# Kernel tuning notes

Hardware: AMD Instinct MI355X
Metric: run time of the kernel (lower is better)

The kernel has to match this reference:

```python
import jax, jax.numpy as jnp
import numpy as np

B, T, D_K, N_HEADS, D_FF, VOCAB, N_LAYERS = 4, 1024, 1024, 16, 4096, 65, 6


def setup_inputs() -> dict:
    key = jax.random.key(0)
    ks = jax.random.split(key, 12)
    f = lambda k, sh: jax.random.normal(k, sh, dtype=jnp.float32) * 0.02
    return {
        "batchData": jax.random.randint(ks[0], (B, T), 0, VOCAB),
        "target": jax.random.randint(ks[1], (B, T), 0, VOCAB),
        "pos": jnp.arange(T),
        "Wtok": f(ks[2], (VOCAB, D_K)),
        "Wpos": f(ks[3], (T, D_K)),
        "Wq": f(ks[4], (D_K, D_K)), "bq": jnp.zeros((D_K,), jnp.float32),
        "Wk": f(ks[5], (D_K, D_K)), "bk": jnp.zeros((D_K,), jnp.float32),
        "Wv": f(ks[6], (D_K, D_K)), "bv": jnp.zeros((D_K,), jnp.float32),
        "W1": f(ks[7], (D_K, D_FF)), "b1": jnp.zeros((D_FF,), jnp.float32),
        "W2": f(ks[8], (D_FF, D_K)), "b2": jnp.zeros((D_K,), jnp.float32),
        "ln_w": jnp.ones((D_K,), jnp.float32),
        "Wf": f(ks[9], (D_K, VOCAB)), "bf": jnp.zeros((VOCAB,), jnp.float32),
        "n_layers": N_LAYERS,
        "n_heads": N_HEADS,
    }


def layer_norm(x, w, eps=1e-5):
    m = jnp.mean(x, axis=-1, keepdims=True)
    v = jnp.var(x, axis=-1, keepdims=True)
    return (x - m) / jnp.sqrt(v + eps) * w


def reference(batchData, target, pos, Wtok, Wpos, Wq, bq, Wk, bk, Wv, bv,
              W1, b1, W2, b2, ln_w, Wf, bf, n_layers, n_heads):
    x = Wtok[batchData] + Wpos[pos]  # [B, T, C] (pos embedding broadcasts)
    Bsz, Tlen, C = x.shape
    dh = C // n_heads
    mask = jnp.tril(jnp.ones((Tlen, Tlen), dtype=bool))
    inv_sqrt_dk = 1.0 / jnp.sqrt(jnp.float32(C))  # source divides by sqrt(full d_k)

    def block(x):
        q = (x @ Wq + bq).reshape(Bsz, Tlen, n_heads, dh).transpose(0, 2, 1, 3)
        k = (x @ Wk + bk).reshape(Bsz, Tlen, n_heads, dh).transpose(0, 2, 1, 3)
        v = (x @ Wv + bv).reshape(Bsz, Tlen, n_heads, dh).transpose(0, 2, 1, 3)
        scores = jnp.einsum('bhqd,bhkd->bhqk', q, k) * inv_sqrt_dk
        scores = jnp.where(mask, scores, -jnp.inf)
        attn = jax.nn.softmax(scores, axis=-1)
        h = jnp.einsum('bhqk,bhkd->bhqd', attn, v)
        h = h.transpose(0, 2, 1, 3).reshape(Bsz, Tlen, C)
        h = h + layer_norm(h, ln_w)           # x = x + ln(x) (shared ln)
        ff = jax.nn.relu(h @ W1 + b1) @ W2 + b2
        return ff + layer_norm(ff, ln_w)      # same shared ln again

    # ModuleList repeats the SAME block object, so weights are shared across layers
    for _ in range(n_layers):
        x = block(x)

    logits = x @ Wf + bf                       # [B, T, V]
    probs = jax.nn.softmax(logits, axis=1)     # softmax over T, as in source
    pred = probs.reshape(Bsz * Tlen, -1)
    onehot = jax.nn.one_hot(target.reshape(-1), VOCAB, dtype=jnp.float32)
    # F.cross_entropy with soft (one-hot float) targets
    loss = -jnp.mean(jnp.sum(onehot * jax.nn.log_softmax(pred, axis=-1), axis=-1))
    return loss, probs
```

## Files before the change

kernel.cpp:

```cpp
#include <hip/hip_runtime.h>

typedef __attribute__((ext_vector_type(8))) short bh8;
typedef __attribute__((ext_vector_type(4))) float f4v;

constexpr int VOC = 65;
constexpr int NL  = 6;
constexpr int Mrow = 4096;

__device__ inline float b2f(unsigned short u) {
  union { unsigned int i; float f; } x; x.i = ((unsigned int)u) << 16; return x.f;
}
__device__ inline unsigned short f2b(float f) {
  union { float f; unsigned int i; } x; x.f = f;
  return (unsigned short)((x.i + 0x7FFFu + ((x.i >> 16) & 1u)) >> 16);
}
__device__ inline unsigned char f2e4m3(float v) {
  return (unsigned char)(__builtin_amdgcn_cvt_pk_fp8_f32(v, v, 0, false) & 0xFF);
}
__device__ inline unsigned int pk4_e4m3(float a, float b, float c, float d) {
  int v = __builtin_amdgcn_cvt_pk_fp8_f32(a, b, 0, false);
  v = __builtin_amdgcn_cvt_pk_fp8_f32(c, d, v, true);
  return (unsigned int)v;
}
__device__ inline void gld16(const void* g, void* l) {
  __builtin_amdgcn_global_load_lds(
      (const __attribute__((address_space(1))) unsigned int*)g,
      (__attribute__((address_space(3))) unsigned int*)l, 16, 0, 0);
}
__device__ inline bh8 lds_swz(const unsigned short* base, int row, int colbyte) {
  int off = row * 128 + (colbyte ^ ((row & 7) << 4));
  return *(const bh8*)((const char*)base + off);
}
__device__ inline f4v mfma16(bh8 a, bh8 b, f4v c) {
  return __builtin_amdgcn_mfma_f32_16x16x32_bf16(a, b, c, 0, 0, 0);
}
__device__ inline f4v mfma8(long a, long b, f4v c) {
  return __builtin_amdgcn_mfma_f32_16x16x32_fp8_fp8(a, b, c, 0, 0, 0);
}
#define WAITV(n) asm volatile("s_waitcnt vmcnt(" #n ")" ::: "memory")
#define LGKM0 asm volatile("s_waitcnt lgkmcnt(0)" ::: "memory")
#define LGKM8 asm volatile("s_waitcnt lgkmcnt(8)" ::: "memory")
#define SBAR0 __builtin_amdgcn_sched_barrier(0)
#define BAR __builtin_amdgcn_s_barrier()

__global__ __launch_bounds__(256) void wt_conv(const float* __restrict__ src,
    unsigned short* __restrict__ dst, int K, int N) {
  __shared__ float t[32][33];
  int k0 = blockIdx.x * 32, n0 = blockIdx.y * 32;
  int tid = threadIdx.x;
#pragma unroll
  for (int i = 0; i < 4; ++i) {
    int idx = tid + i * 256;
    int kr = idx >> 5, nc = idx & 31;
    t[kr][nc] = (n0 + nc < N) ? src[(size_t)(k0 + kr) * N + n0 + nc] : 0.f;
  }
  __syncthreads();
#pragma unroll
  for (int i = 0; i < 4; ++i) {
    int idx = tid + i * 256;
    int nr = idx >> 5, kc = idx & 31;
    dst[(size_t)(n0 + nr) * K + k0 + kc] = f2b(t[kc][nr]);
  }
}

__global__ __launch_bounds__(256) void wt_conv8(const float* __restrict__ src,
    unsigned char* __restrict__ dst, int K, int N) {
  __shared__ float t[32][33];
  int k0 = blockIdx.x * 32, n0 = blockIdx.y * 32;
  int tid = threadIdx.x;
#pragma unroll
  for (int i = 0; i < 4; ++i) {
    int idx = tid + i * 256;
    int kr = idx >> 5, nc = idx & 31;
    t[kr][nc] = (n0 + nc < N) ? src[(size_t)(k0 + kr) * N + n0 + nc] : 0.f;
  }
  __syncthreads();
#pragma unroll
  for (int i = 0; i < 4; ++i) {
    int idx = tid + i * 256;
    int nr = idx >> 5, kc = idx & 31;
    dst[(size_t)(n0 + nr) * K + k0 + kc] = f2e4m3(t[kc][nr] * 16.f);
  }
}

__global__ __launch_bounds__(256) void bias_prep(
    const float* __restrict__ bq, const float* __restrict__ bk,
    const float* __restrict__ bv, const float* __restrict__ bf,
    float* __restrict__ bqkv, float* __restrict__ bfp) {
  int i = blockIdx.x * 256 + threadIdx.x;
  if (i < 1024) bqkv[i] = bq[i];
  else if (i < 2048) bqkv[i] = bk[i - 1024];
  else if (i < 3072) bqkv[i] = bv[i - 2048];
  else if (i < 3200) bfp[i - 3072] = (i - 3072 < VOC) ? bf[i - 3072] : 0.f;
}

__global__ __launch_bounds__(256) void embed_bf(const int* __restrict__ tok,
    const float* __restrict__ Wtok, const float* __restrict__ Wpos,
    unsigned short* __restrict__ Xb) {
  int bt = blockIdx.x, t = bt & 1023, tid = threadIdx.x;
  int id = tok[bt];
  float4 a = ((const float4*)(Wtok + (size_t)id * 1024))[tid];
  float4 p = ((const float4*)(Wpos + (size_t)t * 1024))[tid];
  ushort4 o;
  o.x = f2b(a.x + p.x); o.y = f2b(a.y + p.y);
  o.z = f2b(a.z + p.z); o.w = f2b(a.w + p.w);
  ((ushort4*)(Xb + (size_t)bt * 1024))[tid] = o;
}

template <bool RELU, bool PART, bool VT>
__global__ __launch_bounds__(512, 1) void gemm256(
    const unsigned short* __restrict__ A, const unsigned short* __restrict__ Bt,
    const float* __restrict__ bias, void* __restrict__ Cout,
    unsigned short* __restrict__ Vtout, long N, long Kloop, long lda, long ldb,
    int MT, int NT, int CM, int CN) {
  __shared__ unsigned short Abuf[2][256 * 64];
  __shared__ unsigned short Bbuf[2][256 * 64];
  const int tid = threadIdx.x, lane = tid & 63, w = tid >> 6;
  const int wr = w >> 2, wc = w & 3;
  const int lr = lane & 15, lh = lane >> 4, lh4 = lh * 4;

  const int x = (int)blockIdx.x & 7, j = (int)blockIdx.x >> 3;
  const int gM = MT / CM;
  const int rowT = (x % gM) * CM + (j % CM);
  const int c = (x / gM) * CN + (j / CM);
  const int colT = c % NT, ksl = c / NT;
  const long row0 = (long)rowT * 256, col0 = (long)colT * 256;
  const long kOff = (long)ksl * Kloop;

  f4v acc[8][4];
#pragma unroll
  for (int i = 0; i < 8; ++i)
#pragma unroll
    for (int jj = 0; jj < 4; ++jj) acc[i][jj] = f4v{0.f, 0.f, 0.f, 0.f};

  const int rg = tid >> 3, sIdx = tid & 7;
  const int ch = sIdx ^ (rg & 7);
  const unsigned short* Ap = A + (row0 + rg) * lda + kOff + ch * 8;
  const unsigned short* Bp = Bt + (col0 + rg) * ldb + kOff + ch * 8;

  auto stA = [&](int t, int h) {
    const long k0 = (long)t << 6;
#pragma unroll
    for (int i = 0; i < 2; ++i)
      gld16(Ap + (long)(h * 128 + i * 64) * lda + k0,
            &Abuf[t & 1][(h * 128 + i * 64) * 64 + tid * 8]);
  };
  auto stB = [&](int t, int h) {
    const long k0 = (long)t << 6;
#pragma unroll
    for (int i = 0; i < 2; ++i)
      gld16(Bp + (long)(h * 128 + i * 64) * ldb + k0,
            &Bbuf[t & 1][(h * 128 + i * 64) * 64 + tid * 8]);
  };

  const int nt = (int)(Kloop >> 6);
  stA(0, 0); stA(0, 1); stB(0, 0); stB(0, 1);
  stA(1, 0); stA(1, 1); stB(1, 0);
  WAITV(6);
  BAR;

  const int sl0 = (lh ^ (lr & 7)) * 8;
  const int sl1 = ((4 + lh) ^ (lr & 7)) * 8;

  for (int t = 0; t < nt; ++t) {
    const unsigned short* Ab = Abuf[t & 1];
    const unsigned short* Bb = Bbuf[t & 1];
    bh8 a0[4][2], a1[4][2], b0[2][2], b1[2][2];
#pragma unroll
    for (int mi = 0; mi < 4; ++mi) {
      const int row = (2 * mi + wr) * 16 + lr;
      a0[mi][0] = *(const bh8*)&Ab[row * 64 + sl0];
      a0[mi][1] = *(const bh8*)&Ab[row * 64 + sl1];
    }
#pragma unroll
    for (int ni = 0; ni < 2; ++ni) {
      const int row = (4 * ni + wc) * 16 + lr;
      b0[ni][0] = *(const bh8*)&Bb[row * 64 + sl0];
      b0[ni][1] = *(const bh8*)&Bb[row * 64 + sl1];
    }
    if (t + 1 < nt) stB(t + 1, 1);
    LGKM8;
    BAR;
    LGKM0; SBAR0;
    __builtin_amdgcn_s_setprio(1);
#pragma unroll
    for (int mi = 0; mi < 4; ++mi)
#pragma unroll
      for (int ni = 0; ni < 2; ++ni) {
        acc[mi][ni] = mfma16(a0[mi][0], b0[ni][0], acc[mi][ni]);
        acc[mi][ni] = mfma16(a0[mi][1], b0[ni][1], acc[mi][ni]);
      }
    __builtin_amdgcn_s_setprio(0);
    BAR;
#pragma unroll
    for (int mi = 0; mi < 4; ++mi) {
      const int row = (2 * (mi + 4) + wr) * 16 + lr;
      a1[mi][0] = *(const bh8*)&Ab[row * 64 + sl0];
      a1[mi][1] = *(const bh8*)&Ab[row * 64 + sl1];
    }
    if (t + 2 < nt) stA(t + 2, 0);
    BAR;
    LGKM0; SBAR0;
    __builtin_amdgcn_s_setprio(1);
#pragma unroll
    for (int mi = 0; mi < 4; ++mi)
#pragma unroll
      for (int ni = 0; ni < 2; ++ni) {
        acc[mi + 4][ni] = mfma16(a1[mi][0], b0[ni][0], acc[mi + 4][ni]);
        acc[mi + 4][ni] = mfma16(a1[mi][1], b0[ni][1], acc[mi + 4][ni]);
      }
    __builtin_amdgcn_s_setprio(0);
    BAR;
#pragma unroll
    for (int ni = 0; ni < 2; ++ni) {
      const int row = (4 * (ni + 2) + wc) * 16 + lr;
      b1[ni][0] = *(const bh8*)&Bb[row * 64 + sl0];
      b1[ni][1] = *(const bh8*)&Bb[row * 64 + sl1];
    }
    if (t + 2 < nt) stA(t + 2, 1);
    BAR;
    LGKM0; SBAR0;
    __builtin_amdgcn_s_setprio(1);
#pragma unroll
    for (int mi = 0; mi < 4; ++mi)
#pragma unroll
      for (int ni = 0; ni < 2; ++ni) {
        acc[mi][ni + 2] = mfma16(a0[mi][0], b1[ni][0], acc[mi][ni + 2]);
        acc[mi][ni + 2] = mfma16(a0[mi][1], b1[ni][1], acc[mi][ni + 2]);
      }
    __builtin_amdgcn_s_setprio(0);
    BAR;
    if (t + 2 < nt) stB(t + 2, 0);
    BAR;
    SBAR0;
    __builtin_amdgcn_s_setprio(1);
#pragma unroll
    for (int mi = 0; mi < 4; ++mi)
#pragma unroll
      for (int ni = 0; ni < 2; ++ni) {
        acc[mi + 4][ni + 2] = mfma16(a1[mi][0], b1[ni][0], acc[mi + 4][ni + 2]);
        acc[mi + 4][ni + 2] = mfma16(a1[mi][1], b1[ni][1], acc[mi + 4][ni + 2]);
      }
    __builtin_amdgcn_s_setprio(0);
    if (t + 1 < nt) {
      if (t + 2 < nt) { WAITV(6); } else { WAITV(0); }
      BAR;
    }
  }

  if (PART) {
    unsigned short* P = (unsigned short*)Cout + (size_t)ksl * 4096 * 1024;
#pragma unroll
    for (int mi = 0; mi < 8; ++mi)
#pragma unroll
      for (int ni = 0; ni < 4; ++ni) {
        long col = col0 + (4 * ni + wc) * 16 + lr;
#pragma unroll
        for (int r = 0; r < 4; ++r) {
          long row = row0 + (2 * mi + wr) * 16 + lh4 + r;
          P[row * N + col] = f2b(acc[mi][ni][r]);
        }
      }
    return;
  }
  if (VT && col0 >= 2048) {
#pragma unroll
    for (int mi = 0; mi < 8; ++mi)
#pragma unroll
      for (int ni = 0; ni < 4; ++ni) {
        int col = (int)col0 + (4 * ni + wc) * 16 + lr;
        float bb = bias[col];
        int cc = col - 2048;
        long row = row0 + (2 * mi + wr) * 16 + lh4;
        int bi = (int)(row >> 10), tt = (int)(row & 1023);
        ushort4 o;
        o.x = f2b(acc[mi][ni][0] + bb);
        o.y = f2b(acc[mi][ni][1] + bb);
        o.z = f2b(acc[mi][ni][2] + bb);
        o.w = f2b(acc[mi][ni][3] + bb);
        *(ushort4*)&Vtout[((size_t)(bi * 16 + (cc >> 6)) * 64 + (cc & 63)) *
                              1024 + tt] = o;
      }
    return;
  }
#pragma unroll
  for (int mi = 0; mi < 8; ++mi)
#pragma unroll
    for (int ni = 0; ni < 4; ++ni) {
      long col = col0 + (4 * ni + wc) * 16 + lr;
      float bb = bias[col];
      const float qsc = (VT && col < 1024) ? 0.03125f : 1.0f;
#pragma unroll
      for (int r = 0; r < 4; ++r) {
        long row = row0 + (2 * mi + wr) * 16 + lh4 + r;
        float v = acc[mi][ni][r] + bb;
        if (VT) v *= qsc;
        if (RELU) v = fmaxf(v, 0.f);
        ((unsigned short*)Cout)[row * N + col] = f2b(v);
      }
    }
}

template <bool PART>
__global__ __launch_bounds__(512, 1) void gemm256f8(
    const unsigned char* __restrict__ A, const unsigned char* __restrict__ Bt,
    const float* __restrict__ bias, void* __restrict__ Cout,
    long N, long Kloop, long lda, long ldb, int MT, int NT, int CM, int CN) {
  __shared__ unsigned char Abuf[2][256 * 128];
  __shared__ unsigned char Bbuf[2][256 * 128];
  const int tid = threadIdx.x, lane = tid & 63, w = tid >> 6;
  const int wr = w >> 2, wc = w & 3;
  const int lr = lane & 15, lh = lane >> 4, lh4 = lh * 4;

  const int x = (int)blockIdx.x & 7, j = (int)blockIdx.x >> 3;
  const int gM = MT / CM;
  const int rowT = (x % gM) * CM + (j % CM);
  const int c = (x / gM) * CN + (j / CM);
  const int colT = c % NT, ksl = c / NT;
  const long row0 = (long)rowT * 256, col0 = (long)colT * 256;
  const long kOff = (long)ksl * Kloop;

  f4v acc[8][4];
#pragma unroll
  for (int i = 0; i < 8; ++i)
#pragma unroll
    for (int jj = 0; jj < 4; ++jj) acc[i][jj] = f4v{0.f, 0.f, 0.f, 0.f};

  const int rg = tid >> 3, sIdx = tid & 7;
  const int ch = sIdx ^ (rg & 7);
  const unsigned char* Ap = A + (row0 + rg) * lda + kOff + ch * 16;
  const unsigned char* Bp = Bt + (col0 + rg) * ldb + kOff + ch * 16;

  auto stA = [&](int t, int h) {
    const long k0 = (long)t << 7;
#pragma unroll
    for (int i = 0; i < 2; ++i)
      gld16(Ap + (long)(h * 128 + i * 64) * lda + k0,
            &Abuf[t & 1][(h * 128 + i * 64) * 128 + tid * 16]);
  };
  auto stB = [&](int t, int h) {
    const long k0 = (long)t << 7;
#pragma unroll
    for (int i = 0; i < 2; ++i)
      gld16(Bp + (long)(h * 128 + i * 64) * ldb + k0,
            &Bbuf[t & 1][(h * 128 + i * 64) * 128 + tid * 16]);
  };

  const int nt = (int)(Kloop >> 7);
  stA(0, 0); stA(0, 1); stB(0, 0); stB(0, 1);
  stA(1, 0); stA(1, 1); stB(1, 0);
  WAITV(6);
  BAR;

  int fsl[4];
#pragma unroll
  for (int ks = 0; ks < 4; ++ks)
    fsl[ks] = (((ks * 2 + (lh >> 1)) ^ (lr & 7)) << 4) + (lh & 1) * 8;

  for (int t = 0; t < nt; ++t) {
    const unsigned char* Ab = Abuf[t & 1];
    const unsigned char* Bb = Bbuf[t & 1];
    long a0[4][4], a1[4][4], b0[2][4], b1[2][4];
#pragma unroll
    for (int mi = 0; mi < 4; ++mi) {
      const unsigned char* rp = &Ab[((2 * mi + wr) * 16 + lr) * 128];
#pragma unroll
      for (int ks = 0; ks < 4; ++ks) a0[mi][ks] = *(const long*)&rp[fsl[ks]];
    }
#pragma unroll
    for (int ni = 0; ni < 2; ++ni) {
      const unsigned char* rp = &Bb[((4 * ni + wc) * 16 + lr) * 128];
#pragma unroll
      for (int ks = 0; ks < 4; ++ks) b0[ni][ks] = *(const long*)&rp[fsl[ks]];
    }
    if (t + 1 < nt) stB(t + 1, 1);
    LGKM8;
    BAR;
    LGKM0; SBAR0;
    __builtin_amdgcn_s_setprio(1);
#pragma unroll
    for (int ks = 0; ks < 4; ++ks)
#pragma unroll
      for (int mi = 0; mi < 4; ++mi)
#pragma unroll
        for (int ni = 0; ni < 2; ++ni)
          acc[mi][ni] = mfma8(a0[mi][ks], b0[ni][ks], acc[mi][ni]);
    __builtin_amdgcn_s_setprio(0);
    BAR;
#pragma unroll
    for (int mi = 0; mi < 4; ++mi) {
      const unsigned char* rp = &Ab[((2 * (mi + 4) + wr) * 16 + lr) * 128];
#pragma unroll
      for (int ks = 0; ks < 4; ++ks) a1[mi][ks] = *(const long*)&rp[fsl[ks]];
    }
    if (t + 2 < nt) stA(t + 2, 0);
    BAR;
    LGKM0; SBAR0;
    __builtin_amdgcn_s_setprio(1);
#pragma unroll
    for (int ks = 0; ks < 4; ++ks)
#pragma unroll
      for (int mi = 0; mi < 4; ++mi)
#pragma unroll
        for (int ni = 0; ni < 2; ++ni)
          acc[mi + 4][ni] = mfma8(a1[mi][ks], b0[ni][ks], acc[mi + 4][ni]);
    __builtin_amdgcn_s_setprio(0);
    BAR;
#pragma unroll
    for (int ni = 0; ni < 2; ++ni) {
      const unsigned char* rp = &Bb[((4 * (ni + 2) + wc) * 16 + lr) * 128];
#pragma unroll
      for (int ks = 0; ks < 4; ++ks) b1[ni][ks] = *(const long*)&rp[fsl[ks]];
    }
    if (t + 2 < nt) stA(t + 2, 1);
    BAR;
    LGKM0; SBAR0;
    __builtin_amdgcn_s_setprio(1);
#pragma unroll
    for (int ks = 0; ks < 4; ++ks)
#pragma unroll
      for (int mi = 0; mi < 4; ++mi)
#pragma unroll
        for (int ni = 0; ni < 2; ++ni)
          acc[mi][ni + 2] = mfma8(a0[mi][ks], b1[ni][ks], acc[mi][ni + 2]);
    __builtin_amdgcn_s_setprio(0);
    BAR;
    if (t + 2 < nt) stB(t + 2, 0);
    BAR;
    SBAR0;
    __builtin_amdgcn_s_setprio(1);
#pragma unroll
    for (int ks = 0; ks < 4; ++ks)
#pragma unroll
      for (int mi = 0; mi < 4; ++mi)
#pragma unroll
        for (int ni = 0; ni < 2; ++ni)
          acc[mi + 4][ni + 2] = mfma8(a1[mi][ks], b1[ni][ks], acc[mi + 4][ni + 2]);
    __builtin_amdgcn_s_setprio(0);
    if (t + 1 < nt) {
      if (t + 2 < nt) { WAITV(6); } else { WAITV(0); }
      BAR;
    }
  }

  constexpr float DS = 1.f / 256.f;
  if (PART) {
    unsigned short* P = (unsigned short*)Cout + (size_t)ksl * 4096 * 1024;
#pragma unroll
    for (int mi = 0; mi < 8; ++mi)
#pragma unroll
      for (int ni = 0; ni < 4; ++ni) {
        long col = col0 + (4 * ni + wc) * 16 + lr;
#pragma unroll
        for (int r = 0; r < 4; ++r) {
          long row = row0 + (2 * mi + wr) * 16 + lh4 + r;
          P[row * N + col] = f2b(acc[mi][ni][r] * DS);
        }
      }
    return;
  }
#pragma unroll
  for (int mi = 0; mi < 8; ++mi)
#pragma unroll
    for (int ni = 0; ni < 4; ++ni) {
      long col = col0 + (4 * ni + wc) * 16 + lr;
      float bb = bias[col];
#pragma unroll
      for (int r = 0; r < 4; ++r) {
        long row = row0 + (2 * mi + wr) * 16 + lh4 + r;
        float v = fmaxf(acc[mi][ni][r] * DS + bb, 0.f);
        ((unsigned char*)Cout)[row * N + col] = f2e4m3(v * 16.f);
      }
    }
}

template <int TM, int TN, bool RELU, bool F32OUT>
__global__ __launch_bounds__(256) void gemm4(
    const unsigned short* __restrict__ A, const unsigned short* __restrict__ Bt,
    const float* __restrict__ bias, void* __restrict__ Cout, long N, long K) {
  constexpr int MI = TM / 32, NI = TN / 32;
  constexpr int ABUF = TM * 64, BBUF = TN * 64;
  __shared__ unsigned short As[2 * ABUF];
  __shared__ unsigned short Bs[2 * BBUF];
  const int tid = threadIdx.x;
  const int lane = tid & 63, w = tid >> 6;
  const int wr = w >> 1, wc = w & 1;
  const int lr = lane & 15, lh = lane >> 4, lh4 = lh * 4;
  const long row0 = (long)blockIdx.x * TM, col0 = (long)blockIdx.y * TN;
  f4v acc[MI][NI];
#pragma unroll
  for (int i = 0; i < MI; ++i)
#pragma unroll
    for (int j = 0; j < NI; ++j) acc[i][j] = f4v{0.f, 0.f, 0.f, 0.f};
  const int rg = tid >> 3, s = tid & 7;
  const int ch = s ^ (rg & 7);
  const unsigned short* Ap = A + (row0 + rg) * K + ch * 8;
  const unsigned short* Bp = Bt + (col0 + rg) * K + ch * 8;
  auto stage = [&](int t, int buf) {
    const long k0 = (long)t << 6;
#pragma unroll
    for (int i = 0; i < MI; ++i)
      gld16(Ap + i * 32 * K + k0, &As[buf * ABUF + (i * 256 + tid) * 8]);
#pragma unroll
    for (int i = 0; i < NI; ++i)
      gld16(Bp + i * 32 * K + k0, &Bs[buf * BBUF + (i * 256 + tid) * 8]);
  };
  const int nt = (int)(K >> 6);
  stage(0, 0);
  for (int t = 0; t < nt; ++t) {
    const int cur = t & 1;
    if (t + 1 < nt) {
      stage(t + 1, cur ^ 1);
      WAITV(6);
    } else {
      WAITV(0);
    }
    BAR;
    const unsigned short* Ab = &As[cur * ABUF];
    const unsigned short* Bb = &Bs[cur * BBUF];
#pragma unroll
    for (int ks = 0; ks < 2; ++ks) {
      bh8 a[MI], b[NI];
      const int slot = ((ks << 2) | lh) ^ (lr & 7);
#pragma unroll
      for (int mi = 0; mi < MI; ++mi) {
        int m = wr * (TM / 2) + mi * 16 + lr;
        a[mi] = *(const bh8*)((const char*)Ab + m * 128 + slot * 16);
      }
#pragma unroll
      for (int ni = 0; ni < NI; ++ni) {
        int n = wc * (TN / 2) + ni * 16 + lr;
        b[ni] = *(const bh8*)((const char*)Bb + n * 128 + slot * 16);
      }
#pragma unroll
      for (int mi = 0; mi < MI; ++mi)
#pragma unroll
        for (int ni = 0; ni < NI; ++ni)
          acc[mi][ni] = mfma16(a[mi], b[ni], acc[mi][ni]);
    }
    BAR;
  }
#pragma unroll
  for (int mi = 0; mi < MI; ++mi) {
#pragma unroll
    for (int ni = 0; ni < NI; ++ni) {
      long col = col0 + wc * (TN / 2) + ni * 16 + lr;
      float bb = bias[col];
#pragma unroll
      for (int r = 0; r < 4; ++r) {
        long row = row0 + wr * (TM / 2) + mi * 16 + lh4 + r;
        float v = acc[mi][ni][r] + bb;
        if (RELU) v = fmaxf(v, 0.f);
        if (F32OUT) ((float*)Cout)[row * N + col] = v;
        else ((unsigned short*)Cout)[row * N + col] = f2b(v);
      }
    }
  }
}

__global__ __launch_bounds__(256) void attn_mfma(
    const unsigned short* __restrict__ QKV, const unsigned short* __restrict__ Vt,
    unsigned short* __restrict__ Hout) {
  __shared__ unsigned short Ks[2][64 * 64];
  __shared__ unsigned short Vs[2][64 * 64];
  __shared__ unsigned short Ps[4][16 * 64];
  const int tid = threadIdx.x, w = tid >> 6, lane = tid & 63;
  const int wid = ((int)blockIdx.x & 7) * 128 + ((int)blockIdx.x >> 3);
  const int bh = wid >> 4;
  const int qt = 15 - (wid & 15);
  const int b = bh >> 4, h = bh & 15;
  const int lr = lane & 15, lh = lane >> 4, lh4 = lh * 4;

  const unsigned short* qp =
      QKV + (size_t)(b * 1024 + qt * 64 + w * 16 + lr) * 3072 + h * 64 + lh * 8;
  bh8 aq0 = *(const bh8*)qp;
  bh8 aq1 = *(const bh8*)(qp + 32);

  f4v o[4];
#pragma unroll
  for (int i = 0; i < 4; ++i) o[i] = f4v{0.f, 0.f, 0.f, 0.f};
  float m = -1e30f, l = 0.f;

  const int r8 = tid >> 3, slot = tid & 7;
  unsigned short* pw = &Ps[w][0];

  auto stage = [&](int kt, int buf) {
    int r = r8, c8 = (slot ^ (r & 7)) * 8;
    gld16(QKV + (size_t)(b * 1024 + kt * 64 + r) * 3072 + 1024 + h * 64 + c8,
          &Ks[buf][tid * 8]);
    gld16(Vt + (size_t)(bh * 64 + r) * 1024 + kt * 64 + c8, &Vs[buf][tid * 8]);
    r = r8 + 32; c8 = (slot ^ (r & 7)) * 8;
    gld16(QKV + (size_t)(b * 1024 + kt * 64 + r) * 3072 + 1024 + h * 64 + c8,
          &Ks[buf][2048 + tid * 8]);
    gld16(Vt + (size_t)(bh * 64 + r) * 1024 + kt * 64 + c8,
          &Vs[buf][2048 + tid * 8]);
  };

  stage(0, 0);

  for (int kt = 0; kt <= qt; ++kt) {
    const int cur = kt & 1;
    if (kt < qt) {
      stage(kt + 1, cur ^ 1);
      WAITV(4);
    } else {
      WAITV(0);
    }
    BAR;

    f4v s[4];
#pragma unroll
    for (int nt = 0; nt < 4; ++nt) {
      bh8 k0 = lds_swz(Ks[cur], nt * 16 + lr, lh * 16);
      bh8 k1 = lds_swz(Ks[cur], nt * 16 + lr, lh * 16 + 64);
      f4v z = f4v{0.f, 0.f, 0.f, 0.f};
      z = mfma16(k0, aq0, z);
      z = mfma16(k1, aq1, z);
      s[nt] = z;
    }
    const bool diag = (kt == qt);
    if (diag) {
      const int qloc = w * 16 + lr;
#pragma unroll
      for (int nt = 0; nt < 4; ++nt)
#pragma unroll
        for (int r = 0; r < 4; ++r)
          if ((nt * 16 + lh4 + r) > qloc) s[nt][r] = -1e30f;
    }
    float tm = fmaxf(fmaxf(fmaxf(s[0][0], s[0][1]), fmaxf(s[0][2], s[0][3])),
                     fmaxf(fmaxf(s[1][0], s[1][1]), fmaxf(s[1][2], s[1][3])));
    float tm2 = fmaxf(fmaxf(fmaxf(s[2][0], s[2][1]), fmaxf(s[2][2], s[2][3])),
                      fmaxf(fmaxf(s[3][0], s[3][1]), fmaxf(s[3][2], s[3][3])));
    tm = fmaxf(tm, tm2);
    tm = fmaxf(tm, __shfl_xor(tm, 16));
    tm = fmaxf(tm, __shfl_xor(tm, 32));

    const bool resc = __any(tm > m + 8.f);
    const float mu = resc ? fmaxf(m, tm) : m;
    float sum = 0.f;
#pragma unroll
    for (int nt = 0; nt < 4; ++nt)
#pragma unroll
      for (int r = 0; r < 4; ++r) {
        float e = __expf(s[nt][r] - mu);
        s[nt][r] = e;
        sum += e;
      }
    sum += __shfl_xor(sum, 16);
    sum += __shfl_xor(sum, 32);
    if (resc) {
      float corr = __expf(m - mu);
      m = mu;
      l = l * corr + sum;
      float c0 = __shfl(corr, lh4 + 0), c1 = __shfl(corr, lh4 + 1);
      float c2 = __shfl(corr, lh4 + 2), c3 = __shfl(corr, lh4 + 3);
#pragma unroll
      for (int nt = 0; nt < 4; ++nt) {
        o[nt][0] *= c0; o[nt][1] *= c1; o[nt][2] *= c2; o[nt][3] *= c3;
      }
    } else {
      l += sum;
    }
#pragma unroll
    for (int nt = 0; nt < 4; ++nt) {
      unsigned int u0, u1;
      asm("v_cvt_pk_bf16_f32 %0, %1, %2" : "=v"(u0) : "v"(s[nt][0]), "v"(s[nt][1]));
      asm("v_cvt_pk_bf16_f32 %0, %1, %2" : "=v"(u1) : "v"(s[nt][2]), "v"(s[nt][3]));
      uint2 pk{u0, u1};
      *(uint2*)((char*)pw + lr * 128 + ((nt * 32 + lh * 8) ^ ((lr & 7) << 4))) = pk;
    }
    bh8 pa0 = lds_swz(pw, lr, lh * 16);
    bh8 pa1 = lds_swz(pw, lr, lh * 16 + 64);
#pragma unroll
    for (int nt = 0; nt < 4; ++nt) {
      bh8 v0 = lds_swz(Vs[cur], nt * 16 + lr, lh * 16);
      bh8 v1 = lds_swz(Vs[cur], nt * 16 + lr, lh * 16 + 64);
      o[nt] = mfma16(pa0, v0, o[nt]);
      o[nt] = mfma16(pa1, v1, o[nt]);
    }
    BAR;
  }
  float linv = 1.f / l;
  float l0 = __shfl(linv, lh4 + 0), l1 = __shfl(linv, lh4 + 1);
  float l2 = __shfl(linv, lh4 + 2), l3 = __shfl(linv, lh4 + 3);
  const size_t rowb = (size_t)(b * 1024 + qt * 64 + w * 16);
#pragma unroll
  for (int nt = 0; nt < 4; ++nt) {
    int col = h * 64 + nt * 16 + lr;
    Hout[(rowb + lh4 + 0) * 1024 + col] = f2b(o[nt][0] * l0);
    Hout[(rowb + lh4 + 1) * 1024 + col] = f2b(o[nt][1] * l1);
    Hout[(rowb + lh4 + 2) * 1024 + col] = f2b(o[nt][2] * l2);
    Hout[(rowb + lh4 + 3) * 1024 + col] = f2b(o[nt][3] * l3);
  }
}

template <bool FP8>
__global__ __launch_bounds__(256) void ln_res_bf(
    const unsigned short* __restrict__ Xi, const float* __restrict__ wln,
    void* __restrict__ Y) {
  int row = blockIdx.x, tid = threadIdx.x;
  ushort4 u = ((const ushort4*)(Xi + (size_t)row * 1024))[tid];
  float x0 = b2f(u.x), x1 = b2f(u.y), x2 = b2f(u.z), x3 = b2f(u.w);
  float s = x0 + x1 + x2 + x3;
  float ss = x0 * x0 + x1 * x1 + x2 * x2 + x3 * x3;
#pragma unroll
  for (int off = 32; off; off >>= 1) {
    s += __shfl_xor(s, off);
    ss += __shfl_xor(ss, off);
  }
  __shared__ float sw[4], ssw[4];
  int wv = tid >> 6, ln = tid & 63;
  if (ln == 0) { sw[wv] = s; ssw[wv] = ss; }
  __syncthreads();
  s = sw[0] + sw[1] + sw[2] + sw[3];
  ss = ssw[0] + ssw[1] + ssw[2] + ssw[3];
  float mean = s * (1.f / 1024.f);
  float var = ss * (1.f / 1024.f) - mean * mean;
  float rstd = rsqrtf(var + 1e-5f);
  float4 wv4 = ((const float4*)wln)[tid];
  float y0 = x0 + (x0 - mean) * rstd * wv4.x;
  float y1 = x1 + (x1 - mean) * rstd * wv4.y;
  float y2 = x2 + (x2 - mean) * rstd * wv4.z;
  float y3 = x3 + (x3 - mean) * rstd * wv4.w;
  if (FP8) {
    ((unsigned int*)Y)[row * 256 + tid] =
        pk4_e4m3(y0 * 16.f, y1 * 16.f, y2 * 16.f, y3 * 16.f);
  } else {
    ushort4 out;
    out.x = f2b(y0); out.y = f2b(y1); out.z = f2b(y2); out.w = f2b(y3);
    ((ushort4*)Y)[row * 256 + tid] = out;
  }
}

__global__ __launch_bounds__(256) void ln2_fuse(
    const unsigned short* __restrict__ P, const float* __restrict__ b2,
    const float* __restrict__ wln, unsigned short* __restrict__ Y) {
  int row = blockIdx.x, tid = threadIdx.x;
  const size_t plane = (size_t)4096 * 1024;
  float x0 = 0.f, x1 = 0.f, x2 = 0.f, x3 = 0.f;
#pragma unroll
  for (int pl = 0; pl < 4; ++pl) {
    ushort4 u = *(const ushort4*)&P[pl * plane + (size_t)row * 1024 + tid * 4];
    x0 += b2f(u.x); x1 += b2f(u.y); x2 += b2f(u.z); x3 += b2f(u.w);
  }
  float4 bb = ((const float4*)b2)[tid];
  x0 += bb.x; x1 += bb.y; x2 += bb.z; x3 += bb.w;
  float s = x0 + x1 + x2 + x3;
  float ss = x0 * x0 + x1 * x1 + x2 * x2 + x3 * x3;
#pragma unroll
  for (int off = 32; off; off >>= 1) {
    s += __shfl_xor(s, off);
    ss += __shfl_xor(ss, off);
  }
  __shared__ float sw[4], ssw[4];
  int wv = tid >> 6, ln = tid & 63;
  if (ln == 0) { sw[wv] = s; ssw[wv] = ss; }
  __syncthreads();
  s = sw[0] + sw[1] + sw[2] + sw[3];
  ss = ssw[0] + ssw[1] + ssw[2] + ssw[3];
  float mean = s * (1.f / 1024.f);
  float var = ss * (1.f / 1024.f) - mean * mean;
  float rstd = rsqrtf(var + 1e-5f);
  float4 wv4 = ((const float4*)wln)[tid];
  ushort4 out;
  out.x = f2b(x0 + (x0 - mean) * rstd * wv4.x);
  out.y = f2b(x1 + (x1 - mean) * rstd * wv4.y);
  out.z = f2b(x2 + (x2 - mean) * rstd * wv4.z);
  out.w = f2b(x3 + (x3 - mean) * rstd * wv4.w);
  ((ushort4*)(Y + (size_t)row * 1024))[tid] = out;
}

__global__ __launch_bounds__(256) void softmaxT_kernel(
    const float* __restrict__ logits, float* __restrict__ probs) {
  int b = blockIdx.x / VOC;
  int v = blockIdx.x - b * VOC;
  const float* src = logits + (size_t)b * 1024 * 128 + v;
  float vals[4];
  float m = -1e30f;
#pragma unroll
  for (int i = 0; i < 4; ++i) {
    int t = threadIdx.x + 256 * i;
    vals[i] = src[(size_t)t * 128];
    m = fmaxf(m, vals[i]);
  }
#pragma unroll
  for (int off = 32; off; off >>= 1) m = fmaxf(m, __shfl_xor(m, off));
  __shared__ float sm[4], ssum[4];
  int wv = threadIdx.x >> 6, ln = threadIdx.x & 63;
  if (ln == 0) sm[wv] = m;
  __syncthreads();
  m = fmaxf(fmaxf(sm[0], sm[1]), fmaxf(sm[2], sm[3]));
  float s = 0.f;
#pragma unroll
  for (int i = 0; i < 4; ++i) { vals[i] = __expf(vals[i] - m); s += vals[i]; }
#pragma unroll
  for (int off = 32; off; off >>= 1) s += __shfl_xor(s, off);
  if (ln == 0) ssum[wv] = s;
  __syncthreads();
  s = ssum[0] + ssum[1] + ssum[2] + ssum[3];
  float inv = 1.f / s;
  float* dst = probs + (size_t)b * 1024 * VOC + v;
#pragma unroll
  for (int i = 0; i < 4; ++i) {
    int t = threadIdx.x + 256 * i;
    dst[(size_t)t * VOC] = vals[i] * inv;
  }
}

__global__ __launch_bounds__(256) void loss_rows_kernel(
    const float* __restrict__ probs, const int* __restrict__ tgt,
    float* __restrict__ partial) {
  int wv = threadIdx.x >> 6, lane = threadIdx.x & 63;
  int row = blockIdx.x * 4 + wv;
  const float* p = probs + (size_t)row * VOC;
  float x0 = p[lane];
  float x1 = (lane == 0) ? p[64] : -1e30f;
  float m = fmaxf(x0, x1);
#pragma unroll
  for (int off = 32; off; off >>= 1) m = fmaxf(m, __shfl_xor(m, off));
  float s = __expf(x0 - m) + ((lane == 0) ? __expf(x1 - m) : 0.f);
#pragma unroll
  for (int off = 32; off; off >>= 1) s += __shfl_xor(s, off);
  if (lane == 0) {
    int tg = tgt[row];
    partial[row] = (p[tg] - m) - logf(s);
  }
}

__global__ __launch_bounds__(256) void loss_final_kernel(
    const float* __restrict__ partial, float* __restrict__ out) {
  float s = 0.f;
  for (int i = threadIdx.x; i < Mrow; i += 256) s += partial[i];
#pragma unroll
  for (int off = 32; off; off >>= 1) s += __shfl_xor(s, off);
  __shared__ float sw[4];
  int wv = threadIdx.x >> 6, ln = threadIdx.x & 63;
  if (ln == 0) sw[wv] = s;
  __syncthreads();
  if (threadIdx.x == 0) out[0] = -(sw[0] + sw[1] + sw[2] + sw[3]) / (float)Mrow;
}

extern "C" void kernel_launch(void* const* d_in, const int* in_sizes, int n_in,
                              void* d_out, int out_size, void* d_ws,
                              size_t ws_size, hipStream_t stream) {
  (void)in_sizes; (void)n_in; (void)out_size; (void)ws_size;
  const int*   tok    = (const int*)d_in[0];
  const int*   target = (const int*)d_in[1];
  const float* Wtok   = (const float*)d_in[3];
  const float* Wpos   = (const float*)d_in[4];
  const float* Wq = (const float*)d_in[5];  const float* bq = (const float*)d_in[6];
  const float* Wk = (const float*)d_in[7];  const float* bk = (const float*)d_in[8];
  const float* Wv = (const float*)d_in[9];  const float* bv = (const float*)d_in[10];
  const float* W1 = (const float*)d_in[11]; const float* b1 = (const float*)d_in[12];
  const float* W2 = (const float*)d_in[13]; const float* b2 = (const float*)d_in[14];
  const float* lnw = (const float*)d_in[15];
  const float* Wf = (const float*)d_in[16]; const float* bf = (const float*)d_in[17];
  float* out = (float*)d_out;

  char* p = (char*)d_ws;
  unsigned short* Xb    = (unsigned short*)p; p += (size_t)Mrow * 1024 * 2;
  unsigned short* QKVb  = (unsigned short*)p; p += (size_t)Mrow * 3072 * 2;
  unsigned short* Vt    = (unsigned short*)p; p += (size_t)64 * 64 * 1024 * 2;
  unsigned short* Hb    = (unsigned short*)p; p += (size_t)Mrow * 1024 * 2;
  unsigned char*  F2b8  = (unsigned char*)p;  p += (size_t)Mrow * 1024 * 2;
  unsigned char*  FF1b8 = (unsigned char*)p;  p += (size_t)Mrow * 4096 * 2;
  unsigned short* WqkvT = (unsigned short*)p; p += (size_t)3072 * 1024 * 2;
  unsigned char*  W1T8  = (unsigned char*)p;  p += (size_t)4096 * 1024 * 2;
  unsigned char*  W2T8  = (unsigned char*)p;  p += (size_t)1024 * 4096 * 2;
  unsigned short* WfT   = (unsigned short*)p; p += (size_t)128 * 1024 * 2;
  float* bqkv = (float*)p; p += 3072 * 4;
  float* bfp  = (float*)p; p += 128 * 4;
  float* LOG  = (float*)p; p += (size_t)Mrow * 128 * 4;
  float* PART = (float*)p; p += Mrow * 4;
  unsigned short* Pff2 = QKVb;

  wt_conv<<<dim3(32, 32), 256, 0, stream>>>(Wq, WqkvT,                1024, 1024);
  wt_conv<<<dim3(32, 32), 256, 0, stream>>>(Wk, WqkvT + 1024 * 1024,  1024, 1024);
  wt_conv<<<dim3(32, 32), 256, 0, stream>>>(Wv, WqkvT + 2048 * 1024,  1024, 1024);
  wt_conv8<<<dim3(32, 128), 256, 0, stream>>>(W1, W1T8, 1024, 4096);
  wt_conv8<<<dim3(128, 32), 256, 0, stream>>>(W2, W2T8, 4096, 1024);
  wt_conv<<<dim3(32, 4), 256, 0, stream>>>(Wf, WfT, 1024, VOC);
  bias_prep<<<13, 256, 0, stream>>>(bq, bk, bv, bf, bqkv, bfp);

  embed_bf<<<Mrow, 256, 0, stream>>>(tok, Wtok, Wpos, Xb);

  for (int l = 0; l < NL; ++l) {
    gemm256<false, false, true><<<192, 512, 0, stream>>>(
        Xb, WqkvT, bqkv, QKVb, Vt, 3072, 1024, 1024, 1024, 16, 12, 4, 6);
    attn_mfma<<<1024, 256, 0, stream>>>(QKVb, Vt, Hb);
    ln_res_bf<true><<<Mrow, 256, 0, stream>>>(Hb, lnw, F2b8);
    gemm256f8<false><<<256, 512, 0, stream>>>(
        F2b8, W1T8, b1, FF1b8, 4096, 1024, 1024, 1024, 16, 16, 4, 8);
    gemm256f8<true><<<256, 512, 0, stream>>>(
        FF1b8, W2T8, nullptr, Pff2, 1024, 1024, 4096, 4096, 16, 4, 4, 8);
    ln2_fuse<<<Mrow, 256, 0, stream>>>(Pff2, b2, lnw, Xb);
  }

  gemm4<64, 128, false, true><<<dim3(64, 1), 256, 0, stream>>>(
      Xb, WfT, bfp, LOG, 128, 1024);
  softmaxT_kernel<<<4 * VOC, 256, 0, stream>>>(LOG, out + 1);
  loss_rows_kernel<<<Mrow / 4, 256, 0, stream>>>(out + 1, target, PART);
  loss_final_kernel<<<1, 256, 0, stream>>>(PART, out);
}
```

Baseline: 1.001 ms.

## Enlarge attention tiles to 128 queries and 128 keys per block

Each attention block now handles 128 query rows with 8 waves and iterates over 128-key tiles instead of 64, staging K and two V halves per step. This halves the number of K/V tile loads and barriers per query row, so each staged K/V tile is reused by twice as many queries. In exchange it raises LDS use and register pressure, halves the number of blocks, and wastes more work on masked entries in the diagonal tile.

```diff
diff --git a/kernel.cpp b/kernel.cpp
--- a/kernel.cpp
+++ b/kernel.cpp
@@ -558,21 +558,21 @@
   }
 }
 
-__global__ __launch_bounds__(256) void attn_mfma(
+__global__ __launch_bounds__(512) void attn_mfma(
     const unsigned short* __restrict__ QKV, const unsigned short* __restrict__ Vt,
     unsigned short* __restrict__ Hout) {
-  __shared__ unsigned short Ks[2][64 * 64];
-  __shared__ unsigned short Vs[2][64 * 64];
-  __shared__ unsigned short Ps[4][16 * 64];
+  __shared__ unsigned short Ks[2][128 * 64];
+  __shared__ unsigned short Vs[2][2][64 * 64];
+  __shared__ unsigned short Ps[8][16 * 64];
   const int tid = threadIdx.x, w = tid >> 6, lane = tid & 63;
-  const int wid = ((int)blockIdx.x & 7) * 128 + ((int)blockIdx.x >> 3);
-  const int bh = wid >> 4;
-  const int qt = 15 - (wid & 15);
+  const int wid = ((int)blockIdx.x & 7) * 64 + ((int)blockIdx.x >> 3);
+  const int bh = wid >> 3;
+  const int qt = 7 - (wid & 7);
   const int b = bh >> 4, h = bh & 15;
   const int lr = lane & 15, lh = lane >> 4, lh4 = lh * 4;
 
   const unsigned short* qp =
-      QKV + (size_t)(b * 1024 + qt * 64 + w * 16 + lr) * 3072 + h * 64 + lh * 8;
+      QKV + (size_t)(b * 1024 + qt * 128 + w * 16 + lr) * 3072 + h * 64 + lh * 8;
   bh8 aq0 = *(const bh8*)qp;
   bh8 aq1 = *(const bh8*)(qp + 32);
 
@@ -585,15 +585,16 @@
   unsigned short* pw = &Ps[w][0];
 
   auto stage = [&](int kt, int buf) {
-    int r = r8, c8 = (slot ^ (r & 7)) * 8;
-    gld16(QKV + (size_t)(b * 1024 + kt * 64 + r) * 3072 + 1024 + h * 64 + c8,
+    int c8 = (slot ^ (r8 & 7)) * 8;
+    gld16(QKV + (size_t)(b * 1024 + kt * 128 + r8) * 3072 + 1024 + h * 64 + c8,
           &Ks[buf][tid * 8]);
-    gld16(Vt + (size_t)(bh * 64 + r) * 1024 + kt * 64 + c8, &Vs[buf][tid * 8]);
-    r = r8 + 32; c8 = (slot ^ (r & 7)) * 8;
-    gld16(QKV + (size_t)(b * 1024 + kt * 64 + r) * 3072 + 1024 + h * 64 + c8,
-          &Ks[buf][2048 + tid * 8]);
-    gld16(Vt + (size_t)(bh * 64 + r) * 1024 + kt * 64 + c8,
-          &Vs[buf][2048 + tid * 8]);
+    int r2 = r8 + 64;
+    int c82 = (slot ^ (r2 & 7)) * 8;
+    gld16(QKV + (size_t)(b * 1024 + kt * 128 + r2) * 3072 + 1024 + h * 64 + c82,
+          &Ks[buf][64 * 64 + tid * 8]);
+    gld16(Vt + (size_t)(bh * 64 + r8) * 1024 + kt * 128 + c8, &Vs[buf][0][tid * 8]);
+    gld16(Vt + (size_t)(bh * 64 + r8) * 1024 + kt * 128 + 64 + c8,
+          &Vs[buf][1][tid * 8]);
   };
 
   stage(0, 0);
@@ -608,9 +609,9 @@
     }
     BAR;
 
-    f4v s[4];
-#pragma unroll
-    for (int nt = 0; nt < 4; ++nt) {
+    f4v s[8];
+#pragma unroll
+    for (int nt = 0; nt < 8; ++nt) {
       bh8 k0 = lds_swz(Ks[cur], nt * 16 + lr, lh * 16);
       bh8 k1 = lds_swz(Ks[cur], nt * 16 + lr, lh * 16 + 64);
       f4v z = f4v{0.f, 0.f, 0.f, 0.f};
@@ -618,20 +619,19 @@
       z = mfma16(k1, aq1, z);
       s[nt] = z;
     }
-    const bool diag = (kt == qt);
-    if (diag) {
+    if (kt == qt) {
       const int qloc = w * 16 + lr;
 #pragma unroll
-      for (int nt = 0; nt < 4; ++nt)
+      for (int nt = 0; nt < 8; ++nt)
 #pragma unroll
         for (int r = 0; r < 4; ++r)
           if ((nt * 16 + lh4 + r) > qloc) s[nt][r] = -1e30f;
     }
-    float tm = fmaxf(fmaxf(fmaxf(s[0][0], s[0][1]), fmaxf(s[0][2], s[0][3])),
-                     fmaxf(fmaxf(s[1][0], s[1][1]), fmaxf(s[1][2], s[1][3])));
-    float tm2 = fmaxf(fmaxf(fmaxf(s[2][0], s[2][1]), fmaxf(s[2][2], s[2][3])),
-                      fmaxf(fmaxf(s[3][0], s[3][1]), fmaxf(s[3][2], s[3][3])));
-    tm = fmaxf(tm, tm2);
+    float tm = s[0][0];
+#pragma unroll
+    for (int nt = 0; nt < 8; ++nt)
+#pragma unroll
+      for (int r = 0; r < 4; ++r) tm = fmaxf(tm, s[nt][r]);
     tm = fmaxf(tm, __shfl_xor(tm, 16));
     tm = fmaxf(tm, __shfl_xor(tm, 32));
 
@@ -639,7 +639,7 @@
     const float mu = resc ? fmaxf(m, tm) : m;
     float sum = 0.f;
 #pragma unroll
-    for (int nt = 0; nt < 4; ++nt)
+    for (int nt = 0; nt < 8; ++nt)
 #pragma unroll
       for (int r = 0; r < 4; ++r) {
         float e = __expf(s[nt][r] - mu);
@@ -662,28 +662,33 @@
       l += sum;
     }
 #pragma unroll
-    for (int nt = 0; nt < 4; ++nt) {
-      unsigned int u0, u1;
-      asm("v_cvt_pk_bf16_f32 %0, %1, %2" : "=v"(u0) : "v"(s[nt][0]), "v"(s[nt][1]));
-      asm("v_cvt_pk_bf16_f32 %0, %1, %2" : "=v"(u1) : "v"(s[nt][2]), "v"(s[nt][3]));
-      uint2 pk{u0, u1};
-      *(uint2*)((char*)pw + lr * 128 + ((nt * 32 + lh * 8) ^ ((lr & 7) << 4))) = pk;
-    }
-    bh8 pa0 = lds_swz(pw, lr, lh * 16);
-    bh8 pa1 = lds_swz(pw, lr, lh * 16 + 64);
-#pragma unroll
-    for (int nt = 0; nt < 4; ++nt) {
-      bh8 v0 = lds_swz(Vs[cur], nt * 16 + lr, lh * 16);
-      bh8 v1 = lds_swz(Vs[cur], nt * 16 + lr, lh * 16 + 64);
-      o[nt] = mfma16(pa0, v0, o[nt]);
-      o[nt] = mfma16(pa1, v1, o[nt]);
+    for (int hh = 0; hh < 2; ++hh) {
+#pragma unroll
+      for (int q = 0; q < 4; ++q) {
+        const int nt = hh * 4 + q;
+        unsigned int u0, u1;
+        asm("v_cvt_pk_bf16_f32 %0, %1, %2" : "=v"(u0) : "v"(s[nt][0]), "v"(s[nt][1]));
+        asm("v_cvt_pk_bf16_f32 %0, %1, %2" : "=v"(u1) : "v"(s[nt][2]), "v"(s[nt][3]));
+        uint2 pk{u0, u1};
+        *(uint2*)((char*)pw + lr * 128 + ((q * 32 + lh * 8) ^ ((lr & 7) << 4))) = pk;
+      }
+      bh8 pa0 = lds_swz(pw, lr, lh * 16);
+      bh8 pa1 = lds_swz(pw, lr, lh * 16 + 64);
+      const unsigned short* Vh = Vs[cur][hh];
+#pragma unroll
+      for (int nt2 = 0; nt2 < 4; ++nt2) {
+        bh8 v0 = lds_swz(Vh, nt2 * 16 + lr, lh * 16);
+        bh8 v1 = lds_swz(Vh, nt2 * 16 + lr, lh * 16 + 64);
+        o[nt2] = mfma16(pa0, v0, o[nt2]);
+        o[nt2] = mfma16(pa1, v1, o[nt2]);
+      }
     }
     BAR;
   }
   float linv = 1.f / l;
   float l0 = __shfl(linv, lh4 + 0), l1 = __shfl(linv, lh4 + 1);
   float l2 = __shfl(linv, lh4 + 2), l3 = __shfl(linv, lh4 + 3);
-  const size_t rowb = (size_t)(b * 1024 + qt * 64 + w * 16);
+  const size_t rowb = (size_t)(b * 1024 + qt * 128 + w * 16);
 #pragma unroll
   for (int nt = 0; nt < 4; ++nt) {
     int col = h * 64 + nt * 16 + lr;
@@ -887,7 +892,7 @@
   for (int l = 0; l < NL; ++l) {
     gemm256<false, false, true><<<192, 512, 0, stream>>>(
         Xb, WqkvT, bqkv, QKVb, Vt, 3072, 1024, 1024, 1024, 16, 12, 4, 6);
-    attn_mfma<<<1024, 256, 0, stream>>>(QKVb, Vt, Hb);
+    attn_mfma<<<512, 512, 0, stream>>>(QKVb, Vt, Hb);
     ln_res_bf<true><<<Mrow, 256, 0, stream>>>(Hb, lnw, F2b8);
     gemm256f8<false><<<256, 512, 0, stream>>>(
         F2b8, W1T8, b1, FF1b8, 4096, 1024, 1024, 1024, 16, 16, 4, 8);
```

Measured after the change: 950.0 us. 5.1% less time.
